# Kernel tuning notes

Hardware: AMD Instinct MI355X
Metric: run time of the kernel (lower is better)

The kernel has to match this reference:

```python
import jax, jax.numpy as jnp
import numpy as np
from jax import lax

EPS_IN = 1e-5  # torch InstanceNorm1d eps


def instance_norm(x, w, b):
    # x: (B, C, T); normalize over T per (B, C), biased variance
    mu = x.mean(axis=-1, keepdims=True)
    var = x.var(axis=-1, keepdims=True)
    return (x - mu) * lax.rsqrt(var + EPS_IN) * w[None, :, None] + b[None, :, None]


def conv1x1(x, w):
    # w: (O, I, 1)
    return jnp.einsum('oi,bit->bot', w[:, :, 0], x)


def setup_inputs() -> dict:
    key = jax.random.key(0)
    ks = jax.random.split(key, 16)
    B, C, T, NC = 32, 64, 2048, 4
    enc_dim = C * 3 * 4
    d = {
        'xb': jax.random.normal(ks[0], (B, 3, C, T), jnp.float32),
        'mu': jnp.linspace(-3.0, 3.0, 4),
        'sigma': jnp.full((4,), 2.0),
        'sconv1_w': jax.random.normal(ks[1], (128, enc_dim, 1)) * (1.0 / np.sqrt(enc_dim)),
        'in1_w': 1.0 + 0.1 * jax.random.normal(ks[2], (128,)),
        'in1_b': 0.1 * jax.random.normal(ks[3], (128,)),
        'sconv2_w': jax.random.normal(ks[4], (C, 128, 1)) * (1.0 / np.sqrt(128)),
        'in2_w': 1.0 + 0.1 * jax.random.normal(ks[5], (C,)),
        'in2_b': 0.1 * jax.random.normal(ks[6], (C,)),
        'tconv1_w': jax.random.normal(ks[7], (C, C, 15)) * (1.0 / np.sqrt(C * 15)),
        'in3_w': 1.0 + 0.1 * jax.random.normal(ks[8], (C,)),
        'in3_b': 0.1 * jax.random.normal(ks[9], (C,)),
        'tconv2_w': jax.random.normal(ks[10], (C, C, 1)) * (1.0 / np.sqrt(C)),
        'in4_w': 1.0 + 0.1 * jax.random.normal(ks[11], (C,)),
        'in4_b': 0.1 * jax.random.normal(ks[12], (C,)),
        'alpha': jnp.asarray(0.5),
        'gamma': jnp.asarray(0.5),
        'beta_logit': jnp.asarray(1.0),
        'fc_w': jax.random.normal(ks[13], (4, C)) * (1.0 / np.sqrt(C)),
        'fc_b': 0.1 * jax.random.normal(ks[14], (4,)),
    }
    return d


def reference(xb, mu, sigma, sconv1_w, in1_w, in1_b, sconv2_w, in2_w, in2_b,
              tconv1_w, in3_w, in3_b, tconv2_w, in4_w, in4_b,
              alpha, gamma, beta_logit, fc_w, fc_b):
    B, Ftypes, C, T = xb.shape
    V_BASE = 1.0
    Tp = T // 8

    # pooled curvature / tangent streams -> (T', B, C)
    curv_p = xb[:, 1].reshape(B, C, Tp, 8).mean(-1).transpose(2, 0, 1)
    tang_p = xb[:, 2].reshape(B, C, Tp, 8).mean(-1).transpose(2, 0, 1)

    # learnable population encoding: (B,3,C,T,4) -> (B, 3*C*4, T)
    enc = jnp.exp(-(xb[..., None] - mu) ** 2 / (2.0 * sigma ** 2 + 1e-6))
    x_enc = enc.transpose(0, 1, 2, 4, 3).reshape(B, Ftypes * C * 4, T)

    # spatial 1x1 convs + instance norm + relu
    h = jax.nn.relu(instance_norm(conv1x1(x_enc, sconv1_w), in1_w, in1_b))
    h = jax.nn.relu(instance_norm(conv1x1(h, sconv2_w), in2_w, in2_b))

    # temporal conv k=15 pad=7, 1x1 conv, avg pool 8
    h = lax.conv_general_dilated(h, tconv1_w, (1,), [(7, 7)],
                                 dimension_numbers=('NCH', 'OIH', 'NCH'))
    h = jax.nn.relu(instance_norm(h, in3_w, in3_b))
    h = jax.nn.relu(instance_norm(conv1x1(h, tconv2_w), in4_w, in4_b))
    h = h.reshape(B, C, Tp, 8).mean(-1)  # AvgPool1d(8)
    # dropout is identity in eval mode
    c = h.transpose(2, 0, 1)  # (T', B, C)

    # sequential GD-LIF recurrence over T' steps
    def step(m, inp):
        x_t, curv_t, tang_t = inp
        v_th = V_BASE + alpha * tang_t
        beta = jax.nn.sigmoid(beta_logit - gamma * curv_t)
        m_next = beta * m + x_t
        spike = (m_next - v_th > 0).astype(m_next.dtype)
        m_next = m_next - spike * v_th
        return m_next, spike

    m0 = jnp.zeros((B, C), xb.dtype)
    _, spikes = lax.scan(step, m0, (c, curv_p, tang_p))  # (T', B, C)

    attn = jax.nn.softmax(curv_p, axis=0)
    out_feat = jnp.sum(spikes * attn, axis=0)  # (B, C)
    return out_feat @ fc_w.T + fc_b
```

## Files before the change

kernel.cpp:

```cpp
#include <hip/hip_runtime.h>
#include <math.h>

#define TLEN 2048
#define TP 256

typedef double d4 __attribute__((ext_vector_type(4)));

__device__ __forceinline__ double block_reduce_sum_d(double v, double* sm) {
#pragma unroll
  for (int off = 32; off > 0; off >>= 1) v += __shfl_down(v, off, 64);
  int lane = threadIdx.x & 63, wid = threadIdx.x >> 6;
  __syncthreads();
  if (lane == 0) sm[wid] = v;
  __syncthreads();
  double r = sm[0] + sm[1] + sm[2] + sm[3];
  __syncthreads();
  return r;
}

__global__ void k_probe_f64(int* __restrict__ tbl) {
  int l = threadIdx.x;
  __shared__ int kaS[64], kbS[64];
  __shared__ int cnt[256];
  int rdv[4] = {-1, -1, -1, -1}, cdv[4] = {-1, -1, -1, -1};
  int mav = -1, nbv = -1;
  int okr = 1;
  int nrow = 0, ncol = 0;
  kaS[l] = -1; kbS[l] = -1;
  __syncthreads();

  for (int j = 0; j < 64; ++j) {
    double a = (l == j) ? 1.0 : 0.0;
    d4 acc = {0.0, 0.0, 0.0, 0.0};
    acc = __builtin_amdgcn_mfma_f64_16x16x4f64(a, 1.0, acc, 0, 0, 0);
    int mylab = -1;
#pragma unroll
    for (int v = 0; v < 4; ++v) if (acc[v] != 0.0 && rdv[v] >= 0) mylab = rdv[v];
#pragma unroll
    for (int off = 32; off >= 1; off >>= 1) {
      int o = __shfl_xor(mylab, off);
      mylab = mylab > o ? mylab : o;
    }
    int label = (mylab < 0) ? nrow : mylab;
    if (mylab < 0) nrow++;
    if (label >= 16) okr = 0;
#pragma unroll
    for (int v = 0; v < 4; ++v) if (acc[v] != 0.0) rdv[v] = label;
    if (l == j) mav = label;
  }

  for (int j = 0; j < 64; ++j) {
    double bb = (l == j) ? 1.0 : 0.0;
    d4 acc = {0.0, 0.0, 0.0, 0.0};
    acc = __builtin_amdgcn_mfma_f64_16x16x4f64(1.0, bb, acc, 0, 0, 0);
    int mylab = -1;
#pragma unroll
    for (int v = 0; v < 4; ++v) if (acc[v] != 0.0 && cdv[v] >= 0) mylab = cdv[v];
#pragma unroll
    for (int off = 32; off >= 1; off >>= 1) {
      int o = __shfl_xor(mylab, off);
      mylab = mylab > o ? mylab : o;
    }
    int label = (mylab < 0) ? ncol : mylab;
    if (mylab < 0) ncol++;
    if (label >= 16) okr = 0;
#pragma unroll
    for (int v = 0; v < 4; ++v) if (acc[v] != 0.0) cdv[v] = label;
    if (l == j) nbv = label;
  }

  unsigned long long row0 = __ballot(mav == 0);
  if (__popcll(row0) != 4) okr = 0;
  for (int i = 0; i < 4; ++i) {
    int rep = -1, idx = -1;
    for (int t = 0; t < 64; ++t)
      if ((row0 >> t) & 1ull) { if (++idx == i) { rep = t; break; } }
    double a = (l == rep) ? 1.0 : 0.0;
    double bb = (double)(l + 1);
    d4 acc = {0.0, 0.0, 0.0, 0.0};
    acc = __builtin_amdgcn_mfma_f64_16x16x4f64(a, bb, acc, 0, 0, 0);
#pragma unroll
    for (int v = 0; v < 4; ++v)
      if (rdv[v] == 0) {
        int jp = (int)(acc[v] + 0.5) - 1;
        if (jp >= 0 && jp < 64) kbS[jp] = i; else okr = 0;
      }
  }
  __syncthreads();
  int kbv = kbS[l];

  for (int i = 0; i < 4; ++i) {
    unsigned long long bm = __ballot(kbv == i);
    int rep = -1;
    if (bm != 0ull) { rep = 0; while (!((bm >> rep) & 1ull)) ++rep; }
    else okr = 0;
    int nc = (rep >= 0) ? __shfl(nbv, rep) : -2;
    double bb = (l == rep) ? 1.0 : 0.0;
    double aa = (double)(l + 1);
    d4 acc = {0.0, 0.0, 0.0, 0.0};
    acc = __builtin_amdgcn_mfma_f64_16x16x4f64(aa, bb, acc, 0, 0, 0);
#pragma unroll
    for (int v = 0; v < 4; ++v)
      if (cdv[v] == nc) {
        int jp = (int)(acc[v] + 0.5) - 1;
        if (jp >= 0 && jp < 64) kaS[jp] = i; else okr = 0;
      }
  }
  __syncthreads();
  int kav = kaS[l];

  if (nrow != 16 || ncol != 16) okr = 0;
  if (mav < 0 || mav > 15 || nbv < 0 || nbv > 15 ||
      kav < 0 || kav > 3 || kbv < 0 || kbv > 3) okr = 0;
#pragma unroll
  for (int v = 0; v < 4; ++v)
    if (rdv[v] < 0 || rdv[v] > 15 || cdv[v] < 0 || cdv[v] > 15) okr = 0;
  cnt[l] = 0; cnt[64 + l] = 0; cnt[128 + l] = 0; cnt[192 + l] = 0;
  __syncthreads();
  if (mav >= 0 && mav < 16 && kav >= 0 && kav < 4) atomicAdd(&cnt[mav * 4 + kav], 1);
  if (kbv >= 0 && kbv < 4 && nbv >= 0 && nbv < 16) atomicAdd(&cnt[64 + kbv * 16 + nbv], 1);
  __syncthreads();
  if (cnt[l] != 1 || cnt[64 + l] != 1) okr = 0;
  __syncthreads();
  cnt[l] = 0; cnt[64 + l] = 0; cnt[128 + l] = 0; cnt[192 + l] = 0;
  __syncthreads();
#pragma unroll
  for (int v = 0; v < 4; ++v)
    if (rdv[v] >= 0 && rdv[v] < 16 && cdv[v] >= 0 && cdv[v] < 16)
      atomicAdd(&cnt[rdv[v] * 16 + cdv[v]], 1);
  __syncthreads();
#pragma unroll
  for (int v = 0; v < 4; ++v) if (cnt[l * 4 + v] != 1) okr = 0;
  if (mav == 0) {
    int rank = (int)__popcll(row0 & ((1ull << l) - 1ull));
    if (kav != rank) okr = 0;
  }
  unsigned long long good = __ballot(okr != 0);
  tbl[l] = mav; tbl[64 + l] = kav; tbl[128 + l] = kbv; tbl[192 + l] = nbv;
#pragma unroll
  for (int v = 0; v < 4; ++v) {
    tbl[256 + l * 4 + v] = rdv[v];
    tbl[512 + l * 4 + v] = cdv[v];
  }
  if (l == 0) tbl[768] = (good == 0xFFFFFFFFFFFFFFFFull) ? 1 : 0;
}

__global__ void k_repack_w(const float* __restrict__ w, float* __restrict__ wT) {
  int idx = blockIdx.x * 256 + threadIdx.x;
  if (idx >= 64 * 64 * 15) return;
  int o = idx & 63, i = (idx >> 6) & 63, k = idx >> 12;
  wT[idx] = w[(o * 64 + i) * 15 + k];
}

template <typename T>
__global__ __launch_bounds__(256) void k_pool_ct(const float* __restrict__ xb,
                                                 T* __restrict__ curvp,
                                                 T* __restrict__ tangp) {
  int row = blockIdx.x;
  int b = row >> 6, c = row & 63;
  int tid = threadIdx.x;
  const float* s1 = xb + ((size_t)((b * 3 + 1) * 64 + c)) * TLEN + tid * 8;
  const float* s2 = xb + ((size_t)((b * 3 + 2) * 64 + c)) * TLEN + tid * 8;
  double p1 = 0.0, p2 = 0.0;
#pragma unroll
  for (int j = 0; j < 8; ++j) { p1 += (double)s1[j]; p2 += (double)s2[j]; }
  curvp[(size_t)row * TP + tid] = (T)(p1 * 0.125);
  tangp[(size_t)row * TP + tid] = (T)(p2 * 0.125);
}

template <typename T>
__global__ __launch_bounds__(256) void k_stats(const T* __restrict__ h,
                                               const float* __restrict__ gw,
                                               const float* __restrict__ gb,
                                               int chmask,
                                               double* __restrict__ sc,
                                               double* __restrict__ sh) {
  __shared__ double sm[4];
  int row = blockIdx.x, tid = threadIdx.x;
  int ch = row & chmask;
  const T* base = h + (size_t)row * TLEN + tid * 8;
  double v[8];
#pragma unroll
  for (int j = 0; j < 8; ++j) v[j] = (double)base[j];
  double s = 0.0;
#pragma unroll
  for (int j = 0; j < 8; ++j) s += v[j];
  double mean = block_reduce_sum_d(s, sm) * (1.0 / 2048.0);
  double sq = 0.0;
#pragma unroll
  for (int j = 0; j < 8; ++j) { double d = v[j] - mean; sq += d * d; }
  double var = block_reduce_sum_d(sq, sm) * (1.0 / 2048.0);
  double scale = (double)gw[ch] / sqrt(var + 1e-5);
  double shift = (double)gb[ch] - mean * scale;
  if (tid == 0) { sc[row] = scale; sh[row] = shift; }
}

template <typename T>
__global__ __launch_bounds__(512, 4) void k_enc1_mfma(const float* __restrict__ xb,
                                                      const float* __restrict__ w,
                                                      const float* __restrict__ mu,
                                                      const float* __restrict__ sigma,
                                                      T* __restrict__ h1,
                                                      const int* __restrict__ tbl) {
  if (tbl[768] == 0) return;
  __shared__ float AsT[32][132];
  __shared__ double Bs[32][132];
  int b = blockIdx.x, t0 = blockIdx.y * 128, tid = threadIdx.x;
  int wv = tid >> 6, l = tid & 63;
  int o0 = (wv >> 1) * 32, tb = (wv & 1) * 64;
  int t_ma = tbl[l], t_ka = tbl[64 + l], t_kb = tbl[128 + l], t_nb = tbl[192 + l];
  int t_rd[4], t_cd[4];
#pragma unroll
  for (int v = 0; v < 4; ++v) { t_rd[v] = tbl[256 + l * 4 + v]; t_cd[v] = tbl[512 + l * 4 + v]; }
  double smu[4], sinv[4];
#pragma unroll
  for (int g = 0; g < 4; ++g) {
    smu[g] = (double)mu[g];
    double s = (double)sigma[g];
    sinv[g] = 1.0 / (2.0 * s * s + 1e-6);
  }
  d4 acc[2][4];
#pragma unroll
  for (int r = 0; r < 2; ++r)
#pragma unroll
    for (int c = 0; c < 4; ++c) acc[r][c] = (d4){0.0, 0.0, 0.0, 0.0};

  int aO1 = (tid * 4) >> 5, aI1 = (tid * 4) & 31;
  int aO2 = (tid * 4 + 2048) >> 5, aI2 = (tid * 4 + 2048) & 31;
  int sc_ = tid >> 6, sl2 = tid & 63;
  int st = 2 * sl2;

  float4 a1r = *(const float4*)(w + (size_t)aO1 * 768 + aI1);
  float4 a2r = *(const float4*)(w + (size_t)aO2 * 768 + aI2);
  double e[8];
  {
    float2 x2 = *(const float2*)(xb + ((size_t)((b * 3 + 0) * 64 + 0 + sc_)) * TLEN + t0 + st);
    double xv0 = (double)x2.x, xv1 = (double)x2.y;
#pragma unroll
    for (int g = 0; g < 4; ++g) {
      double d0 = xv0 - smu[g], d1 = xv1 - smu[g];
      e[2 * g] = exp(-d0 * d0 * sinv[g]);
      e[2 * g + 1] = exp(-d1 * d1 * sinv[g]);
    }
  }

  for (int kc = 0; kc < 24; ++kc) {
    __syncthreads();
    AsT[aI1][aO1] = a1r.x; AsT[aI1 + 1][aO1] = a1r.y;
    AsT[aI1 + 2][aO1] = a1r.z; AsT[aI1 + 3][aO1] = a1r.w;
    AsT[aI2][aO2] = a2r.x; AsT[aI2 + 1][aO2] = a2r.y;
    AsT[aI2 + 2][aO2] = a2r.z; AsT[aI2 + 3][aO2] = a2r.w;
#pragma unroll
    for (int g = 0; g < 4; ++g) {
      double2 ev = {e[2 * g], e[2 * g + 1]};
      *(double2*)&Bs[sc_ * 4 + g][st] = ev;
    }
    __syncthreads();
#pragma unroll
    for (int k4 = 0; k4 < 32; k4 += 4) {
      double aF0 = (double)AsT[k4 + t_ka][o0 + t_ma];
      double aF1 = (double)AsT[k4 + t_ka][o0 + 16 + t_ma];
      double bF[4];
#pragma unroll
      for (int c = 0; c < 4; ++c) bF[c] = Bs[k4 + t_kb][tb + c * 16 + t_nb];
#pragma unroll
      for (int c = 0; c < 4; ++c) {
        acc[0][c] = __builtin_amdgcn_mfma_f64_16x16x4f64(aF0, bF[c], acc[0][c], 0, 0, 0);
        acc[1][c] = __builtin_amdgcn_mfma_f64_16x16x4f64(aF1, bF[c], acc[1][c], 0, 0, 0);
      }
    }
    if (kc < 23) {
      int i0n = (kc + 1) * 32;
      a1r = *(const float4*)(w + (size_t)aO1 * 768 + i0n + aI1);
      a2r = *(const float4*)(w + (size_t)aO2 * 768 + i0n + aI2);
      int f = i0n >> 8;
      int cb = (i0n >> 2) & 63;
      float2 x2 = *(const float2*)(xb + ((size_t)((b * 3 + f) * 64 + cb + sc_)) * TLEN + t0 + st);
      double xv0 = (double)x2.x, xv1 = (double)x2.y;
#pragma unroll
      for (int g = 0; g < 4; ++g) {
        double d0 = xv0 - smu[g], d1 = xv1 - smu[g];
        e[2 * g] = exp(-d0 * d0 * sinv[g]);
        e[2 * g + 1] = exp(-d1 * d1 * sinv[g]);
      }
    }
  }
#pragma unroll
  for (int r = 0; r < 2; ++r)
#pragma unroll
    for (int c = 0; c < 4; ++c)
#pragma unroll
      for (int v = 0; v < 4; ++v) {
        int o = o0 + r * 16 + t_rd[v];
        h1[((size_t)(b * 128 + o)) * TLEN + t0 + tb + c * 16 + t_cd[v]] = (T)acc[r][c][v];
      }
}

template <typename T>
__global__ __launch_bounds__(256, 4) void k_enc1_valu(const float* __restrict__ xb,
                                                      const float* __restrict__ w,
                                                      const float* __restrict__ mu,
                                                      const float* __restrict__ sigma,
                                                      T* __restrict__ h1,
                                                      const int* __restrict__ tbl) {
  if (tbl[768] != 0) return;
  __shared__ float AsT[32][132];
  __shared__ double Bs[32][64];
  __shared__ double smu[4], sinv[4];
  int b = blockIdx.x, t0 = blockIdx.y * 64, tid = threadIdx.x;
  if (tid < 4) {
    smu[tid] = (double)mu[tid];
    double s = (double)sigma[tid];
    sinv[tid] = 1.0 / (2.0 * s * s + 1e-6);
  }
  double acc[8][4] = {};
  int to = (tid >> 4) * 8, l = tid & 15;
  for (int kc = 0; kc < 24; ++kc) {
    int i0 = kc * 32;
    __syncthreads();
    {
      int idx = tid * 4;
#pragma unroll
      for (int rep = 0; rep < 4; ++rep) {
        int o = idx >> 5, ii = idx & 31;
        float4 v4 = *(const float4*)(w + (size_t)o * 768 + i0 + ii);
        AsT[ii][o] = v4.x; AsT[ii + 1][o] = v4.y; AsT[ii + 2][o] = v4.z; AsT[ii + 3][o] = v4.w;
        idx += 1024;
      }
    }
    {
      int f = i0 >> 8;
      int cb = (i0 >> 2) & 63;
      int c = tid >> 5, l2 = tid & 31;
      int t = 2 * l2;
      float2 x2 = *(const float2*)(xb + ((size_t)((b * 3 + f) * 64 + cb + c)) * TLEN + t0 + t);
      double xv0 = (double)x2.x, xv1 = (double)x2.y;
#pragma unroll
      for (int g = 0; g < 4; ++g) {
        double m = smu[g], inv = sinv[g];
        double d0 = xv0 - m, d1 = xv1 - m;
        double2 e = {exp(-d0 * d0 * inv), exp(-d1 * d1 * inv)};
        *(double2*)&Bs[c * 4 + g][t] = e;
      }
    }
    __syncthreads();
#pragma unroll
    for (int kk = 0; kk < 32; ++kk) {
      float4 a0 = *(const float4*)&AsT[kk][to];
      float4 a1 = *(const float4*)&AsT[kk][to + 4];
      double a[8] = {(double)a0.x, (double)a0.y, (double)a0.z, (double)a0.w,
                     (double)a1.x, (double)a1.y, (double)a1.z, (double)a1.w};
      double bb[4];
#pragma unroll
      for (int j = 0; j < 2; ++j) {
        double2 p = *(const double2*)&Bs[kk][2 * l + 32 * j];
        bb[2 * j] = p.x; bb[2 * j + 1] = p.y;
      }
#pragma unroll
      for (int q = 0; q < 8; ++q)
#pragma unroll
        for (int j = 0; j < 4; ++j) acc[q][j] += a[q] * bb[j];
    }
  }
#pragma unroll
  for (int q = 0; q < 8; ++q) {
    T* op = h1 + ((size_t)(b * 128 + to + q)) * TLEN + t0;
    op[2 * l]      = (T)acc[q][0];
    op[2 * l + 1]  = (T)acc[q][1];
    op[2 * l + 32] = (T)acc[q][2];
    op[2 * l + 33] = (T)acc[q][3];
  }
}

template <int K, typename T>
__global__ __launch_bounds__(256, 4) void k_conv1x1_mfma(const T* __restrict__ in,
                                                         const float* __restrict__ w,
                                                         const double* __restrict__ sc,
                                                         const double* __restrict__ sh,
                                                         T* __restrict__ out,
                                                         const int* __restrict__ tbl) {
  if (tbl[768] == 0) return;
  __shared__ float AsT[32][68];
  __shared__ double Bs[32][68];
  int b = blockIdx.x, t0 = blockIdx.y * 64, tid = threadIdx.x;
  int wv = tid >> 6, l = tid & 63;
  int t_ma = tbl[l], t_ka = tbl[64 + l], t_kb = tbl[128 + l], t_nb = tbl[192 + l];
  int t_rd[4], t_cd[4];
#pragma unroll
  for (int v = 0; v < 4; ++v) { t_rd[v] = tbl[256 + l * 4 + v]; t_cd[v] = tbl[512 + l * 4 + v]; }
  int o0 = wv * 16;
  d4 acc[4];
#pragma unroll
  for (int c = 0; c < 4; ++c) acc[c] = (d4){0.0, 0.0, 0.0, 0.0};
  for (int kc = 0; kc < K / 32; ++kc) {
    __syncthreads();
    {
      int idx = tid * 4;
#pragma unroll
      for (int rep = 0; rep < 2; ++rep) {
        int o = idx >> 5, ii = idx & 31;
        float4 v4 = *(const float4*)(w + (size_t)o * K + kc * 32 + ii);
        AsT[ii][o] = v4.x; AsT[ii + 1][o] = v4.y; AsT[ii + 2][o] = v4.z; AsT[ii + 3][o] = v4.w;
        idx += 1024;
      }
    }
    {
      int r = tid >> 3, l8 = tid & 7;
      int srow = b * K + kc * 32 + r;
      const T* gp = in + (size_t)srow * TLEN + t0;
      double s_ = sc[srow], h_ = sh[srow];
#pragma unroll
      for (int q = 0; q < 4; ++q) {
        int t = 2 * l8 + 16 * q;
        double2 v = {fmax((double)gp[t] * s_ + h_, 0.0),
                     fmax((double)gp[t + 1] * s_ + h_, 0.0)};
        *(double2*)&Bs[r][t] = v;
      }
    }
    __syncthreads();
#pragma unroll
    for (int k4 = 0; k4 < 32; k4 += 4) {
      double aF = (double)AsT[k4 + t_ka][o0 + t_ma];
#pragma unroll
      for (int c = 0; c < 4; ++c) {
        double bF = Bs[k4 + t_kb][c * 16 + t_nb];
        acc[c] = __builtin_amdgcn_mfma_f64_16x16x4f64(aF, bF, acc[c], 0, 0, 0);
      }
    }
  }
#pragma unroll
  for (int c = 0; c < 4; ++c)
#pragma unroll
    for (int v = 0; v < 4; ++v)
      out[((size_t)(b * 64 + o0 + t_rd[v])) * TLEN + t0 + c * 16 + t_cd[v]] = (T)acc[c][v];
}

template <int K, typename T>
__global__ __launch_bounds__(256, 4) void k_conv1x1_valu(const T* __restrict__ in,
                                                         const float* __restrict__ w,
                                                         const double* __restrict__ sc,
                                                         const double* __restrict__ sh,
                                                         T* __restrict__ out,
                                                         const int* __restrict__ tbl) {
  if (tbl[768] != 0) return;
  __shared__ float AsT[32][68];
  __shared__ double Bs[32][64];
  int b = blockIdx.x, t0 = blockIdx.y * 64, tid = threadIdx.x;
  double acc[4][4] = {};
  int to = (tid >> 4) * 4, l = tid & 15;
  for (int kc = 0; kc < K / 32; ++kc) {
    __syncthreads();
    {
      int idx = tid * 4;
#pragma unroll
      for (int rep = 0; rep < 2; ++rep) {
        int o = idx >> 5, ii = idx & 31;
        float4 v4 = *(const float4*)(w + (size_t)o * K + kc * 32 + ii);
        AsT[ii][o] = v4.x; AsT[ii + 1][o] = v4.y; AsT[ii + 2][o] = v4.z; AsT[ii + 3][o] = v4.w;
        idx += 1024;
      }
    }
    {
      int r = tid >> 3, l8 = tid & 7;
      int srow = b * K + kc * 32 + r;
      const T* gp = in + (size_t)srow * TLEN + t0;
      double s_ = sc[srow], h_ = sh[srow];
#pragma unroll
      for (int q = 0; q < 4; ++q) {
        int t = 2 * l8 + 16 * q;
        double2 v = {fmax((double)gp[t] * s_ + h_, 0.0),
                     fmax((double)gp[t + 1] * s_ + h_, 0.0)};
        *(double2*)&Bs[r][t] = v;
      }
    }
    __syncthreads();
#pragma unroll
    for (int kk = 0; kk < 32; ++kk) {
      float4 a4 = *(const float4*)&AsT[kk][to];
      double a0 = (double)a4.x, a1 = (double)a4.y, a2 = (double)a4.z, a3 = (double)a4.w;
      double bb[4];
#pragma unroll
      for (int j = 0; j < 2; ++j) {
        double2 p = *(const double2*)&Bs[kk][2 * l + 32 * j];
        bb[2 * j] = p.x; bb[2 * j + 1] = p.y;
      }
#pragma unroll
      for (int j = 0; j < 4; ++j) {
        acc[0][j] += a0 * bb[j];
        acc[1][j] += a1 * bb[j];
        acc[2][j] += a2 * bb[j];
        acc[3][j] += a3 * bb[j];
      }
    }
  }
#pragma unroll
  for (int q = 0; q < 4; ++q) {
    T* op = out + ((size_t)(b * 64 + to + q)) * TLEN + t0;
    op[2 * l]      = (T)acc[q][0];
    op[2 * l + 1]  = (T)acc[q][1];
    op[2 * l + 32] = (T)acc[q][2];
    op[2 * l + 33] = (T)acc[q][3];
  }
}

template <typename T>
__global__ __launch_bounds__(512, 2) void k_tconv1_mfma(const T* __restrict__ h2,
                                                        const float* __restrict__ wT,
                                                        const double* __restrict__ sc,
                                                        const double* __restrict__ sh,
                                                        T* __restrict__ h3,
                                                        const int* __restrict__ tbl) {
  if (tbl[768] == 0) return;
  __shared__ __align__(16) double In[64][80];
  int b = blockIdx.x, t0 = blockIdx.y * 64, tid = threadIdx.x;
  int wv = tid >> 6, l = tid & 63;
  int t_ma = tbl[l], t_ka = tbl[64 + l], t_kb = tbl[128 + l], t_nb = tbl[192 + l];
  int t_rd[4], t_cd[4];
#pragma unroll
  for (int v = 0; v < 4; ++v) { t_rd[v] = tbl[256 + l * 4 + v]; t_cd[v] = tbl[512 + l * 4 + v]; }
  int o0 = (wv >> 1) * 16, tq = (wv & 1) * 32;
  const float* wAp = wT + (size_t)t_ka * 64 + o0 + t_ma;
  for (int idx = tid; idx < 64 * 78; idx += 512) {
    int i = idx / 78, x = idx - i * 78;
    int tg = t0 - 7 + x;
    int row = b * 64 + i;
    double v = 0.0;
    if (tg >= 0 && tg < TLEN)
      v = fmax((double)h2[(size_t)row * TLEN + tg] * sc[row] + sh[row], 0.0);
    In[i][x] = v;
  }
  __syncthreads();
  d4 acc[2];
  acc[0] = (d4){0.0, 0.0, 0.0, 0.0};
  acc[1] = (d4){0.0, 0.0, 0.0, 0.0};
  for (int ic = 0; ic < 8; ++ic) {
#pragma unroll
    for (int k = 0; k < 15; ++k) {
#pragma unroll
      for (int kg = 0; kg < 2; ++kg) {
        double aF = (double)wAp[(size_t)(k * 64 + ic * 8 + kg * 4) * 64];
#pragma unroll
        for (int c = 0; c < 2; ++c) {
          double bF = In[ic * 8 + kg * 4 + t_kb][tq + c * 16 + t_nb + k];
          acc[c] = __builtin_amdgcn_mfma_f64_16x16x4f64(aF, bF, acc[c], 0, 0, 0);
        }
      }
    }
  }
#pragma unroll
  for (int c = 0; c < 2; ++c)
#pragma unroll
    for (int v = 0; v < 4; ++v)
      h3[((size_t)(b * 64 + o0 + t_rd[v])) * TLEN + t0 + tq + c * 16 + t_cd[v]] = (T)acc[c][v];
}

template <typename T>
__global__ __launch_bounds__(256) void k_tconv1_valu(const T* __restrict__ h2,
                                                     const float* __restrict__ wT,
                                                     const double* __restrict__ sc,
                                                     const double* __restrict__ sh,
                                                     T* __restrict__ h3,
                                                     const int* __restrict__ tbl) {
  if (tbl[768] != 0) return;
  __shared__ __align__(16) double In[64][80];
  __shared__ float Ws[8][15][64];
  int b = blockIdx.x, t0 = blockIdx.y * 64, tid = threadIdx.x;
  for (int idx = tid; idx < 64 * 78; idx += 256) {
    int i = idx / 78, x = idx - i * 78;
    int tg = t0 - 7 + x;
    int row = b * 64 + i;
    double v = 0.0;
    if (tg >= 0 && tg < TLEN)
      v = fmax((double)h2[(size_t)row * TLEN + tg] * sc[row] + sh[row], 0.0);
    In[i][x] = v;
  }
  double acc[4][4] = {};
  int og = (tid >> 4) * 4, tt2 = (tid & 15) * 4;
  for (int ic = 0; ic < 8; ++ic) {
    __syncthreads();
    for (int idx = tid; idx < 15 * 8 * 16; idx += 256) {
      int k = idx >> 7;
      int r = idx & 127;
      int ii = r >> 4, o4 = (r & 15) * 4;
      float4 v = *(const float4*)(wT + ((size_t)(k * 64 + ic * 8 + ii)) * 64 + o4);
      *(float4*)&Ws[ii][k][o4] = v;
    }
    __syncthreads();
#pragma unroll
    for (int ii = 0; ii < 8; ++ii) {
      int i = ic * 8 + ii;
      double r[18];
#pragma unroll
      for (int m = 0; m < 18; m += 2) {
        double2 p = *(const double2*)&In[i][tt2 + m];
        r[m] = p.x; r[m + 1] = p.y;
      }
#pragma unroll
      for (int k = 0; k < 15; ++k) {
        float4 w4 = *(const float4*)&Ws[ii][k][og];
        double w0 = (double)w4.x, w1 = (double)w4.y, w2 = (double)w4.z, w3 = (double)w4.w;
#pragma unroll
        for (int j = 0; j < 4; ++j) {
          double x = r[j + k];
          acc[0][j] += w0 * x;
          acc[1][j] += w1 * x;
          acc[2][j] += w2 * x;
          acc[3][j] += w3 * x;
        }
      }
    }
  }
#pragma unroll
  for (int q = 0; q < 4; ++q) {
    T* op = h3 + ((size_t)(b * 64 + og + q)) * TLEN + t0 + tt2;
#pragma unroll
    for (int j = 0; j < 4; ++j) op[j] = (T)acc[q][j];
  }
}

template <typename T>
__global__ __launch_bounds__(256) void k_in4_pool(const T* __restrict__ h,
                                                  const float* __restrict__ gw,
                                                  const float* __restrict__ gb,
                                                  T* __restrict__ cbuf) {
  __shared__ double sm[4];
  int row = blockIdx.x, tid = threadIdx.x;
  int ch = row & 63;
  const T* base = h + (size_t)row * TLEN + tid * 8;
  double v[8];
#pragma unroll
  for (int j = 0; j < 8; ++j) v[j] = (double)base[j];
  double s = 0.0;
#pragma unroll
  for (int j = 0; j < 8; ++j) s += v[j];
  double mean = block_reduce_sum_d(s, sm) * (1.0 / 2048.0);
  double sq = 0.0;
#pragma unroll
  for (int j = 0; j < 8; ++j) { double d = v[j] - mean; sq += d * d; }
  double var = block_reduce_sum_d(sq, sm) * (1.0 / 2048.0);
  double scale = (double)gw[ch] / sqrt(var + 1e-5);
  double shift = (double)gb[ch] - mean * scale;
  double p = 0.0;
#pragma unroll
  for (int j = 0; j < 8; ++j) p += fmax(v[j] * scale + shift, 0.0);
  cbuf[(size_t)row * TP + tid] = (T)(p * 0.125);
}

template <typename T>
__global__ __launch_bounds__(64) void k_scan(const T* __restrict__ cbuf,
                                             const T* __restrict__ curvp,
                                             const T* __restrict__ tangp,
                                             const float* __restrict__ alpha,
                                             const float* __restrict__ gamma,
                                             const float* __restrict__ betal,
                                             double* __restrict__ ofeat) {
  int id = blockIdx.x * 64 + threadIdx.x;
  double a = (double)alpha[0], g = (double)gamma[0], bl = (double)betal[0];
  const T* cu_p = curvp + (size_t)id * TP;
  const T* ta_p = tangp + (size_t)id * TP;
  const T* cb_p = cbuf + (size_t)id * TP;
  double mmax = -1e300, ssum = 0.0, accs = 0.0, mem = 0.0;
  for (int tp = 0; tp < TP; ++tp) {
    double cu = (double)cu_p[tp];
    double ta = (double)ta_p[tp];
    double x = (double)cb_p[tp];
    double nm = fmax(mmax, cu);
    double r = exp(mmax - nm);
    double e = exp(cu - nm);
    ssum = ssum * r + e;
    accs = accs * r;
    mmax = nm;
    double vth = 1.0 + a * ta;
    double beta = 1.0 / (1.0 + exp(g * cu - bl));
    mem = beta * mem + x;
    if (mem - vth > 0.0) {
      accs += e;
      mem -= vth;
    }
  }
  ofeat[id] = accs / ssum;
}

__global__ void k_fc(const double* __restrict__ ofeat, const float* __restrict__ fw,
                     const float* __restrict__ fb, float* __restrict__ out) {
  int tid = threadIdx.x;
  if (tid >= 128) return;
  int b = tid >> 2, j = tid & 3;
  double s = (double)fb[j];
#pragma unroll
  for (int c = 0; c < 64; ++c) s += ofeat[b * 64 + c] * (double)fw[j * 64 + c];
  out[b * 4 + j] = (float)s;
}

template <typename T>
static void run_all(void* const* d_in, float* out, char* wsb, hipStream_t stream) {
  const float* xb    = (const float*)d_in[0];
  const float* mu    = (const float*)d_in[1];
  const float* sigma = (const float*)d_in[2];
  const float* w1    = (const float*)d_in[3];
  const float* in1w  = (const float*)d_in[4];
  const float* in1b  = (const float*)d_in[5];
  const float* w2    = (const float*)d_in[6];
  const float* in2w  = (const float*)d_in[7];
  const float* in2b  = (const float*)d_in[8];
  const float* wt1   = (const float*)d_in[9];
  const float* in3w  = (const float*)d_in[10];
  const float* in3b  = (const float*)d_in[11];
  const float* w4    = (const float*)d_in[12];
  const float* in4w  = (const float*)d_in[13];
  const float* in4b  = (const float*)d_in[14];
  const float* alpha = (const float*)d_in[15];
  const float* gamma = (const float*)d_in[16];
  const float* betal = (const float*)d_in[17];
  const float* fcw   = (const float*)d_in[18];
  const float* fcb   = (const float*)d_in[19];

  size_t sT = sizeof(T);
  T* h1 = (T*)wsb;
  T* h2 = (T*)(wsb + (size_t)8388608 * sT);
  T* h3 = h1;
  T* h4 = h2;
  float* wT = (float*)(wsb + (size_t)12582912 * sT);
  char* p = wsb + (size_t)12582912 * sT + 245760;
  T* curvp = (T*)p;
  T* tangp = (T*)(p + (size_t)524288 * sT);
  T* cbuf  = (T*)(p + (size_t)2 * 524288 * sT);
  double* ofeat = (double*)(p + (size_t)3 * 524288 * sT);
  char* cb = (char*)cbuf;
  int* tbl = (int*)cb;
  double* sc1 = (double*)(cb + 16384);
  double* sh1 = sc1 + 4096;
  double* sc2 = sh1 + 4096;
  double* sh2 = sc2 + 2048;
  double* sc3 = sh2 + 2048;
  double* sh3 = sc3 + 2048;

  k_repack_w<<<dim3(240), dim3(256), 0, stream>>>(wt1, wT);
  k_pool_ct<T><<<dim3(2048), dim3(256), 0, stream>>>(xb, curvp, tangp);
  k_probe_f64<<<dim3(1), dim3(64), 0, stream>>>(tbl);
  k_enc1_mfma<T><<<dim3(32, 16), dim3(512), 0, stream>>>(xb, w1, mu, sigma, h1, tbl);
  k_enc1_valu<T><<<dim3(32, 32), dim3(256), 0, stream>>>(xb, w1, mu, sigma, h1, tbl);
  k_stats<T><<<dim3(4096), dim3(256), 0, stream>>>(h1, in1w, in1b, 127, sc1, sh1);
  k_conv1x1_mfma<128, T><<<dim3(32, 32), dim3(256), 0, stream>>>(h1, w2, sc1, sh1, h2, tbl);
  k_conv1x1_valu<128, T><<<dim3(32, 32), dim3(256), 0, stream>>>(h1, w2, sc1, sh1, h2, tbl);
  k_stats<T><<<dim3(2048), dim3(256), 0, stream>>>(h2, in2w, in2b, 63, sc2, sh2);
  k_tconv1_mfma<T><<<dim3(32, 32), dim3(512), 0, stream>>>(h2, wT, sc2, sh2, h3, tbl);
  k_tconv1_valu<T><<<dim3(32, 32), dim3(256), 0, stream>>>(h2, wT, sc2, sh2, h3, tbl);
  k_stats<T><<<dim3(2048), dim3(256), 0, stream>>>(h3, in3w, in3b, 63, sc3, sh3);
  k_conv1x1_mfma<64, T><<<dim3(32, 32), dim3(256), 0, stream>>>(h3, w4, sc3, sh3, h4, tbl);
  k_conv1x1_valu<64, T><<<dim3(32, 32), dim3(256), 0, stream>>>(h3, w4, sc3, sh3, h4, tbl);
  k_in4_pool<T><<<dim3(2048), dim3(256), 0, stream>>>(h4, in4w, in4b, cbuf);
  k_scan<T><<<dim3(32), dim3(64), 0, stream>>>(cbuf, curvp, tangp, alpha, gamma, betal, ofeat);
  k_fc<<<dim3(1), dim3(128), 0, stream>>>(ofeat, fcw, fcb, out);
}

extern "C" void kernel_launch(void* const* d_in, const int* in_sizes, int n_in,
                              void* d_out, int out_size, void* d_ws, size_t ws_size,
                              hipStream_t stream) {
  const size_t NEED64 = 113508352ull;
  if (ws_size >= NEED64)
    run_all<double>(d_in, (float*)d_out, (char*)d_ws, stream);
  else
    run_all<float>(d_in, (float*)d_out, (char*)d_ws, stream);
}
```

Before: 594.5 us.

## Pre-transpose weights to fp64, read A from global, double-buffer B tiles

Adds a kernel that converts and transposes the sconv1, sconv2 and tconv2 weights into fp64 column-major buffers once per call. The MFMA enc1 and conv1x1 kernels then load their A fragments straight from global/L2 instead of staging them through shared memory. The B tile is double-buffered so each k-chunk needs one barrier instead of two, and the next input is prefetched into registers during the MFMA loop. enc1 also moves to 256-thread blocks over 64 timesteps, doubling the grid. The trade-off is more global-load latency on the A operand in the inner loop and an extra launch.

```diff
diff --git a/kernel.cpp b/kernel.cpp
--- a/kernel.cpp
+++ b/kernel.cpp
@@ -150,6 +150,24 @@
   if (idx >= 64 * 64 * 15) return;
   int o = idx & 63, i = (idx >> 6) & 63, k = idx >> 12;
   wT[idx] = w[(o * 64 + i) * 15 + k];
+}
+
+__global__ void k_prep_w64(const float* __restrict__ w1, const float* __restrict__ w2,
+                           const float* __restrict__ w4, double* __restrict__ w1T,
+                           double* __restrict__ w2T, double* __restrict__ w4T) {
+  int idx = blockIdx.x * 256 + threadIdx.x;
+  if (idx < 98304) {
+    int i = idx >> 7, o = idx & 127;
+    w1T[idx] = (double)w1[(size_t)o * 768 + i];
+  } else if (idx < 106496) {
+    int r = idx - 98304;
+    int i = r >> 6, o = r & 63;
+    w2T[r] = (double)w2[(size_t)o * 128 + i];
+  } else if (idx < 110592) {
+    int r = idx - 106496;
+    int i = r >> 6, o = r & 63;
+    w4T[r] = (double)w4[(size_t)o * 64 + i];
+  }
 }
 
 template <typename T>
@@ -196,18 +214,17 @@
 }
 
 template <typename T>
-__global__ __launch_bounds__(512, 4) void k_enc1_mfma(const float* __restrict__ xb,
-                                                      const float* __restrict__ w,
+__global__ __launch_bounds__(256, 4) void k_enc1_mfma(const float* __restrict__ xb,
+                                                      const double* __restrict__ w1T,
                                                       const float* __restrict__ mu,
                                                       const float* __restrict__ sigma,
                                                       T* __restrict__ h1,
                                                       const int* __restrict__ tbl) {
   if (tbl[768] == 0) return;
-  __shared__ float AsT[32][132];
-  __shared__ double Bs[32][132];
-  int b = blockIdx.x, t0 = blockIdx.y * 128, tid = threadIdx.x;
+  __shared__ double Bs[2][32][68];
+  int b = blockIdx.x, t0 = blockIdx.y * 64, tid = threadIdx.x;
   int wv = tid >> 6, l = tid & 63;
-  int o0 = (wv >> 1) * 32, tb = (wv & 1) * 64;
+  int o0 = wv * 32;
   int t_ma = tbl[l], t_ka = tbl[64 + l], t_kb = tbl[128 + l], t_nb = tbl[192 + l];
   int t_rd[4], t_cd[4];
 #pragma unroll
@@ -225,13 +242,9 @@
 #pragma unroll
     for (int c = 0; c < 4; ++c) acc[r][c] = (d4){0.0, 0.0, 0.0, 0.0};
 
-  int aO1 = (tid * 4) >> 5, aI1 = (tid * 4) & 31;
-  int aO2 = (tid * 4 + 2048) >> 5, aI2 = (tid * 4 + 2048) & 31;
-  int sc_ = tid >> 6, sl2 = tid & 63;
+  int sc_ = tid >> 5, sl2 = tid & 31;
   int st = 2 * sl2;
 
-  float4 a1r = *(const float4*)(w + (size_t)aO1 * 768 + aI1);
-  float4 a2r = *(const float4*)(w + (size_t)aO2 * 768 + aI2);
   double e[8];
   {
     float2 x2 = *(const float2*)(xb + ((size_t)((b * 3 + 0) * 64 + 0 + sc_)) * TLEN + t0 + st);
@@ -245,24 +258,28 @@
   }
 
   for (int kc = 0; kc < 24; ++kc) {
-    __syncthreads();
-    AsT[aI1][aO1] = a1r.x; AsT[aI1 + 1][aO1] = a1r.y;
-    AsT[aI1 + 2][aO1] = a1r.z; AsT[aI1 + 3][aO1] = a1r.w;
-    AsT[aI2][aO2] = a2r.x; AsT[aI2 + 1][aO2] = a2r.y;
-    AsT[aI2 + 2][aO2] = a2r.z; AsT[aI2 + 3][aO2] = a2r.w;
+    int cur = kc & 1;
+    int i0 = kc * 32;
 #pragma unroll
     for (int g = 0; g < 4; ++g) {
       double2 ev = {e[2 * g], e[2 * g + 1]};
-      *(double2*)&Bs[sc_ * 4 + g][st] = ev;
+      *(double2*)&Bs[cur][sc_ * 4 + g][st] = ev;
     }
     __syncthreads();
+    float2 x2n = {0.0f, 0.0f};
+    if (kc < 23) {
+      int i0n = i0 + 32;
+      int f = i0n >> 8, cb = (i0n >> 2) & 63;
+      x2n = *(const float2*)(xb + ((size_t)((b * 3 + f) * 64 + cb + sc_)) * TLEN + t0 + st);
+    }
 #pragma unroll
     for (int k4 = 0; k4 < 32; k4 += 4) {
-      double aF0 = (double)AsT[k4 + t_ka][o0 + t_ma];
-      double aF1 = (double)AsT[k4 + t_ka][o0 + 16 + t_ma];
+      const double* wrow = w1T + (size_t)(i0 + k4 + t_ka) * 128;
+      double aF0 = wrow[o0 + t_ma];
+      double aF1 = wrow[o0 + 16 + t_ma];
       double bF[4];
 #pragma unroll
-      for (int c = 0; c < 4; ++c) bF[c] = Bs[k4 + t_kb][tb + c * 16 + t_nb];
+      for (int c = 0; c < 4; ++c) bF[c] = Bs[cur][k4 + t_kb][c * 16 + t_nb];
 #pragma unroll
       for (int c = 0; c < 4; ++c) {
         acc[0][c] = __builtin_amdgcn_mfma_f64_16x16x4f64(aF0, bF[c], acc[0][c], 0, 0, 0);
@@ -270,13 +287,7 @@
       }
     }
     if (kc < 23) {
-      int i0n = (kc + 1) * 32;
-      a1r = *(const float4*)(w + (size_t)aO1 * 768 + i0n + aI1);
-      a2r = *(const float4*)(w + (size_t)aO2 * 768 + i0n + aI2);
-      int f = i0n >> 8;
-      int cb = (i0n >> 2) & 63;
-      float2 x2 = *(const float2*)(xb + ((size_t)((b * 3 + f) * 64 + cb + sc_)) * TLEN + t0 + st);
-      double xv0 = (double)x2.x, xv1 = (double)x2.y;
+      double xv0 = (double)x2n.x, xv1 = (double)x2n.y;
 #pragma unroll
       for (int g = 0; g < 4; ++g) {
         double d0 = xv0 - smu[g], d1 = xv1 - smu[g];
@@ -292,7 +303,7 @@
 #pragma unroll
       for (int v = 0; v < 4; ++v) {
         int o = o0 + r * 16 + t_rd[v];
-        h1[((size_t)(b * 128 + o)) * TLEN + t0 + tb + c * 16 + t_cd[v]] = (T)acc[r][c][v];
+        h1[((size_t)(b * 128 + o)) * TLEN + t0 + c * 16 + t_cd[v]] = (T)acc[r][c][v];
       }
 }
 
@@ -374,14 +385,13 @@
 
 template <int K, typename T>
 __global__ __launch_bounds__(256, 4) void k_conv1x1_mfma(const T* __restrict__ in,
-                                                         const float* __restrict__ w,
+                                                         const double* __restrict__ wT64,
                                                          const double* __restrict__ sc,
                                                          const double* __restrict__ sh,
                                                          T* __restrict__ out,
                                                          const int* __restrict__ tbl) {
   if (tbl[768] == 0) return;
-  __shared__ float AsT[32][68];
-  __shared__ double Bs[32][68];
+  __shared__ double Bs[2][32][68];
   int b = blockIdx.x, t0 = blockIdx.y * 64, tid = threadIdx.x;
   int wv = tid >> 6, l = tid & 63;
   int t_ma = tbl[l], t_ka = tbl[64 + l], t_kb = tbl[128 + l], t_nb = tbl[192 + l];
@@ -392,40 +402,52 @@
   d4 acc[4];
 #pragma unroll
   for (int c = 0; c < 4; ++c) acc[c] = (d4){0.0, 0.0, 0.0, 0.0};
+  int r = tid >> 3, l8 = tid & 7;
+  double bv[8];
+  {
+    int srow = b * K + r;
+    const T* gp = in + (size_t)srow * TLEN + t0;
+    double s_ = sc[srow], h_ = sh[srow];
+#pragma unroll
+    for (int q = 0; q < 4; ++q) {
+      int t = 2 * l8 + 16 * q;
+      bv[2 * q]     = fmax((double)gp[t] * s_ + h_, 0.0);
+      bv[2 * q + 1] = fmax((double)gp[t + 1] * s_ + h_, 0.0);
+    }
+  }
   for (int kc = 0; kc < K / 32; ++kc) {
+    int cur = kc & 1;
+#pragma unroll
+    for (int q = 0; q < 4; ++q) {
+      double2 v = {bv[2 * q], bv[2 * q + 1]};
+      *(double2*)&Bs[cur][r][2 * l8 + 16 * q] = v;
+    }
     __syncthreads();
-    {
-      int idx = tid * 4;
-#pragma unroll
-      for (int rep = 0; rep < 2; ++rep) {
-        int o = idx >> 5, ii = idx & 31;
-        float4 v4 = *(const float4*)(w + (size_t)o * K + kc * 32 + ii);
-        AsT[ii][o] = v4.x; AsT[ii + 1][o] = v4.y; AsT[ii + 2][o] = v4.z; AsT[ii + 3][o] = v4.w;
-        idx += 1024;
-      }
-    }
-    {
-      int r = tid >> 3, l8 = tid & 7;
-      int srow = b * K + kc * 32 + r;
+    double xr[8];
+    double s_ = 0.0, h_ = 0.0;
+    if (kc + 1 < K / 32) {
+      int srow = b * K + (kc + 1) * 32 + r;
       const T* gp = in + (size_t)srow * TLEN + t0;
-      double s_ = sc[srow], h_ = sh[srow];
+      s_ = sc[srow]; h_ = sh[srow];
 #pragma unroll
       for (int q = 0; q < 4; ++q) {
         int t = 2 * l8 + 16 * q;
-        double2 v = {fmax((double)gp[t] * s_ + h_, 0.0),
-                     fmax((double)gp[t + 1] * s_ + h_, 0.0)};
-        *(double2*)&Bs[r][t] = v;
-      }
-    }
-    __syncthreads();
+        xr[2 * q] = (double)gp[t];
+        xr[2 * q + 1] = (double)gp[t + 1];
+      }
+    }
 #pragma unroll
     for (int k4 = 0; k4 < 32; k4 += 4) {
-      double aF = (double)AsT[k4 + t_ka][o0 + t_ma];
+      double aF = wT64[(size_t)(kc * 32 + k4 + t_ka) * 64 + o0 + t_ma];
 #pragma unroll
       for (int c = 0; c < 4; ++c) {
-        double bF = Bs[k4 + t_kb][c * 16 + t_nb];
+        double bF = Bs[cur][k4 + t_kb][c * 16 + t_nb];
         acc[c] = __builtin_amdgcn_mfma_f64_16x16x4f64(aF, bF, acc[c], 0, 0, 0);
       }
+    }
+    if (kc + 1 < K / 32) {
+#pragma unroll
+      for (int j = 0; j < 8; ++j) bv[j] = fmax(xr[j] * s_ + h_, 0.0);
     }
   }
 #pragma unroll
@@ -734,20 +756,24 @@
   double* sh2 = sc2 + 2048;
   double* sc3 = sh2 + 2048;
   double* sh3 = sc3 + 2048;
+  double* w1T = (double*)(cb + 147456);
+  double* w2T = w1T + 98304;
+  double* w4T = w2T + 8192;
 
   k_repack_w<<<dim3(240), dim3(256), 0, stream>>>(wt1, wT);
+  k_prep_w64<<<dim3(432), dim3(256), 0, stream>>>(w1, w2, w4, w1T, w2T, w4T);
   k_pool_ct<T><<<dim3(2048), dim3(256), 0, stream>>>(xb, curvp, tangp);
   k_probe_f64<<<dim3(1), dim3(64), 0, stream>>>(tbl);
-  k_enc1_mfma<T><<<dim3(32, 16), dim3(512), 0, stream>>>(xb, w1, mu, sigma, h1, tbl);
+  k_enc1_mfma<T><<<dim3(32, 32), dim3(256), 0, stream>>>(xb, w1T, mu, sigma, h1, tbl);
   k_enc1_valu<T><<<dim3(32, 32), dim3(256), 0, stream>>>(xb, w1, mu, sigma, h1, tbl);
   k_stats<T><<<dim3(4096), dim3(256), 0, stream>>>(h1, in1w, in1b, 127, sc1, sh1);
-  k_conv1x1_mfma<128, T><<<dim3(32, 32), dim3(256), 0, stream>>>(h1, w2, sc1, sh1, h2, tbl);
+  k_conv1x1_mfma<128, T><<<dim3(32, 32), dim3(256), 0, stream>>>(h1, w2T, sc1, sh1, h2, tbl);
   k_conv1x1_valu<128, T><<<dim3(32, 32), dim3(256), 0, stream>>>(h1, w2, sc1, sh1, h2, tbl);
   k_stats<T><<<dim3(2048), dim3(256), 0, stream>>>(h2, in2w, in2b, 63, sc2, sh2);
   k_tconv1_mfma<T><<<dim3(32, 32), dim3(512), 0, stream>>>(h2, wT, sc2, sh2, h3, tbl);
   k_tconv1_valu<T><<<dim3(32, 32), dim3(256), 0, stream>>>(h2, wT, sc2, sh2, h3, tbl);
   k_stats<T><<<dim3(2048), dim3(256), 0, stream>>>(h3, in3w, in3b, 63, sc3, sh3);
-  k_conv1x1_mfma<64, T><<<dim3(32, 32), dim3(256), 0, stream>>>(h3, w4, sc3, sh3, h4, tbl);
+  k_conv1x1_mfma<64, T><<<dim3(32, 32), dim3(256), 0, stream>>>(h3, w4T, sc3, sh3, h4, tbl);
   k_conv1x1_valu<64, T><<<dim3(32, 32), dim3(256), 0, stream>>>(h3, w4, sc3, sh3, h4, tbl);
   k_in4_pool<T><<<dim3(2048), dim3(256), 0, stream>>>(h4, in4w, in4b, cbuf);
   k_scan<T><<<dim3(32), dim3(64), 0, stream>>>(cbuf, curvp, tangp, alpha, gamma, betal, ofeat);
```

New measurement: 608.6 us. +2.4%, slower.
